# Kernel tuning notes

Hardware: AMD Instinct MI355X
Metric: run time of the kernel (lower is better)

Reference implementation:

```python
import jax, jax.numpy as jnp
import numpy as np

B, NCLASS, NSUPP = 4096, 1000, 64
NCHUNK = NSUPP * NSUPP  # 4096, x's feature dim


def setup_inputs() -> dict:
    key = jax.random.key(0)
    k1, k2, k3 = jax.random.split(key, 3)
    x = jax.random.normal(k1, (B, NCHUNK), dtype=jnp.float32)
    # torch .uniform_(-1, 1)
    wSupp = jax.random.uniform(k2, (NCLASS, NSUPP), dtype=jnp.float32, minval=-1.0, maxval=1.0)
    chunk_map = jax.random.randint(k3, (NCLASS, NSUPP), 0, NCHUNK, dtype=jnp.int32)
    return {"x": x, "wSupp": wSupp, "chunk_map": chunk_map}


def reference(x, wSupp, chunk_map):
    # sparse_support: for each class i, feat_i = sum_j x[:, chunk_map[i,j]] * wSupp[i,j]; out = exp(feat)
    gathered = x[:, chunk_map]                      # [B, nClass, nSupp] gather via index map
    feats = jnp.einsum('bcs,cs->bc', gathered, wSupp)  # weighted sum over support
    return jnp.exp(feats)                           # [B, nClass]
```

## Files before the change

### kernel.cpp

```cpp
#include <hip/hip_runtime.h>
#include <hip/hip_fp16.h>


constexpr int B_       = 4096;
constexpr int NCLASS_  = 1000;
constexpr int NSUPP_   = 64;
constexpr int NCHUNK_  = 4096;
constexpr int BT       = 8;
constexpr int THREADS_ = 1024;
constexpr int SG_      = NSUPP_ / 4;
constexpr size_t CMT_BYTES = (size_t)SG_ * NCLASS_ * 16;
constexpr size_t WS_NEEDED = 2 * CMT_BYTES;

__global__ __launch_bounds__(256)
void build_cw_kernel(const int*   __restrict__ cm,
                     const float* __restrict__ w,
                     int*         __restrict__ cmT,
                     __half2*     __restrict__ wTh)
{
    const int t    = threadIdx.x;
    const int c    = blockIdx.x * 4 + (t >> 6);
    const int lane = t & 63;
    if (c >= NCLASS_) return;

    const int   idx = cm[c * NSUPP_ + lane];
    const float wv  = w [c * NSUPP_ + lane];
    const int   key = (idx - c) & 7;

    const unsigned long long below = ((unsigned long long)1 << lane) - 1ull;
    int j = 0;
    #pragma unroll
    for (int r = 0; r < 8; ++r) {
        const unsigned long long m = __ballot(key == r);
        if (key > r)  j += __popcll(m);
        if (key == r) j += __popcll(m & below);
    }

    const int dst = ((j >> 2) * NCLASS_ + c) * 4 + (j & 3);
    cmT[dst] = idx;
    wTh[dst] = __float2half2_rn(wv);
}

static __device__ __forceinline__ __half2 f2h2(const float u) {
    union U { float f; __half2 h; } uu;
    uu.f = u;
    return uu.h;
}
static __device__ __forceinline__ float h2f(const __half2 h) {
    union U { __half2 h; float f; } uu;
    uu.h = h;
    return uu.f;
}

#define GSUPP(d, wj)                               \
    a0 = __hfma2(f2h2((d).x), (wj), a0);           \
    a1 = __hfma2(f2h2((d).y), (wj), a1);           \
    a2 = __hfma2(f2h2((d).z), (wj), a2);           \
    a3 = __hfma2(f2h2((d).w), (wj), a3);

#define FLUSH_ACC() {                              \
    float2 t_;                                     \
    t_ = __half22float2(a0); f0x += t_.x; f0y += t_.y; \
    t_ = __half22float2(a1); f1x += t_.x; f1y += t_.y; \
    t_ = __half22float2(a2); f2x += t_.x; f2y += t_.y; \
    t_ = __half22float2(a3); f3x += t_.x; f3y += t_.y; \
    a0 = z_; a1 = z_; a2 = z_; a3 = z_; }

template <bool USET>
__global__ __launch_bounds__(THREADS_)
void supp_gather_kernel(const float* __restrict__ x,
                        const float* __restrict__ wSupp,
                        const int*   __restrict__ cmap,
                        const float4* __restrict__ wTh4,
                        const int4*   __restrict__ cmT,
                        float*       __restrict__ out)
{
    __shared__ __align__(16) __half2 tile[NCHUNK_ * 4];

    const int t  = threadIdx.x;
    const int rb = blockIdx.x * BT;

    #pragma unroll
    for (int p = 0; p < NCHUNK_ / THREADS_; ++p) {
        const size_t col = (size_t)t + THREADS_ * p;
        float v0 = x[(size_t)(rb + 0) * NCHUNK_ + col];
        float v1 = x[(size_t)(rb + 1) * NCHUNK_ + col];
        float v2 = x[(size_t)(rb + 2) * NCHUNK_ + col];
        float v3 = x[(size_t)(rb + 3) * NCHUNK_ + col];
        float v4 = x[(size_t)(rb + 4) * NCHUNK_ + col];
        float v5 = x[(size_t)(rb + 5) * NCHUNK_ + col];
        float v6 = x[(size_t)(rb + 6) * NCHUNK_ + col];
        float v7 = x[(size_t)(rb + 7) * NCHUNK_ + col];
        float4 pk;
        pk.x = h2f(__floats2half2_rn(v0, v1));
        pk.y = h2f(__floats2half2_rn(v2, v3));
        pk.z = h2f(__floats2half2_rn(v4, v5));
        pk.w = h2f(__floats2half2_rn(v6, v7));
        *reinterpret_cast<float4*>(&tile[col * 4]) = pk;
    }
    __syncthreads();

    if (t < NCLASS_) {
        const int c = t;
        const float4* tile4 = reinterpret_cast<const float4*>(tile);

        const __half2 z_ = __floats2half2_rn(0.f, 0.f);
        __half2 a0 = z_, a1 = z_, a2 = z_, a3 = z_;
        float f0x = 0.f, f0y = 0.f, f1x = 0.f, f1y = 0.f;
        float f2x = 0.f, f2y = 0.f, f3x = 0.f, f3y = 0.f;

        int4   ci;
        float4 wh;
        if constexpr (USET) {
            ci = cmT [c];
            wh = wTh4[c];
        } else {
            ci = reinterpret_cast<const int4*>(cmap + c * NSUPP_)[0];
            wh = reinterpret_cast<const float4*>(wSupp + c * NSUPP_)[0];
        }

        #pragma unroll
        for (int sg = 0; sg < SG_; ++sg) {
            const int4   c4 = ci;
            const float4 w4 = wh;

            const int sgn = (sg + 1 < SG_) ? sg + 1 : SG_ - 1;
            if constexpr (USET) {
                ci = cmT [sgn * NCLASS_ + c];
                wh = wTh4[sgn * NCLASS_ + c];
            } else {
                ci = reinterpret_cast<const int4*>(cmap + c * NSUPP_)[sgn];
                wh = reinterpret_cast<const float4*>(wSupp + c * NSUPP_)[sgn];
            }

            const float4 d0 = tile4[c4.x];
            const float4 d1 = tile4[c4.y];
            const float4 d2 = tile4[c4.z];
            const float4 d3 = tile4[c4.w];

            const __half2 w0 = USET ? f2h2(w4.x) : __float2half2_rn(w4.x);
            const __half2 w1 = USET ? f2h2(w4.y) : __float2half2_rn(w4.y);
            const __half2 w2 = USET ? f2h2(w4.z) : __float2half2_rn(w4.z);
            const __half2 w3 = USET ? f2h2(w4.w) : __float2half2_rn(w4.w);

            GSUPP(d0, w0)
            GSUPP(d1, w1)
            GSUPP(d2, w2)
            GSUPP(d3, w3)

            if ((sg & 3) == 3) { FLUSH_ACC() }
        }

        out[(size_t)(rb + 0) * NCLASS_ + c] = __expf(f0x);
        out[(size_t)(rb + 1) * NCLASS_ + c] = __expf(f0y);
        out[(size_t)(rb + 2) * NCLASS_ + c] = __expf(f1x);
        out[(size_t)(rb + 3) * NCLASS_ + c] = __expf(f1y);
        out[(size_t)(rb + 4) * NCLASS_ + c] = __expf(f2x);
        out[(size_t)(rb + 5) * NCLASS_ + c] = __expf(f2y);
        out[(size_t)(rb + 6) * NCLASS_ + c] = __expf(f3x);
        out[(size_t)(rb + 7) * NCLASS_ + c] = __expf(f3y);
    }
}

extern "C" void kernel_launch(void* const* d_in, const int* in_sizes, int n_in,
                              void* d_out, int out_size, void* d_ws, size_t ws_size,
                              hipStream_t stream) {
    const float* x  = (const float*)d_in[0];
    const float* w  = (const float*)d_in[1];
    const int*   cm = (const int*)d_in[2];
    float*       o  = (float*)d_out;

    int*     cmT = (int*)d_ws;
    __half2* wTh = (__half2*)((char*)d_ws + CMT_BYTES);

    const dim3 grid(B_ / BT);
    if (ws_size >= WS_NEEDED) {
        build_cw_kernel<<<dim3((NCLASS_ + 3) / 4), dim3(256), 0, stream>>>(
            cm, w, cmT, wTh);
        supp_gather_kernel<true><<<grid, dim3(THREADS_), 0, stream>>>(
            x, w, cm, (const float4*)wTh, (const int4*)cmT, o);
    } else {
        supp_gather_kernel<false><<<grid, dim3(THREADS_), 0, stream>>>(
            x, w, cm, (const float4*)wTh, (const int4*)cmT, o);
    }
}
```

Baseline: 111.6 us.

## Process two row-tiles per block, overlapping second tile load with first gather

Each block now handles 16 batch rows as two 8-row halves held in a double-sized LDS tile. Global loads for the second half are issued between gather steps of the first half, with sched_barriers pinning the interleave, so memory latency overlaps the LDS gather and FMA work. Index and weight prefetch is reorganised into two ping-pong register sets, and the idle threads (t >= 1000) now also run the gather. The grid halves, LDS use doubles to 128KB per block, and register pressure rises, which may hurt occupancy.

```diff
diff --git a/kernel.cpp b/kernel.cpp
--- a/kernel.cpp
+++ b/kernel.cpp
@@ -6,7 +6,7 @@
 constexpr int NCLASS_  = 1000;
 constexpr int NSUPP_   = 64;
 constexpr int NCHUNK_  = 4096;
-constexpr int BT       = 8;
+constexpr int BT       = 16;
 constexpr int THREADS_ = 1024;
 constexpr int SG_      = NSUPP_ / 4;
 constexpr size_t CMT_BYTES = (size_t)SG_ * NCLASS_ * 16;
@@ -52,11 +52,43 @@
     return uu.f;
 }
 
+#define SB() __builtin_amdgcn_sched_barrier(0)
+
 #define GSUPP(d, wj)                               \
     a0 = __hfma2(f2h2((d).x), (wj), a0);           \
     a1 = __hfma2(f2h2((d).y), (wj), a1);           \
     a2 = __hfma2(f2h2((d).z), (wj), a2);           \
     a3 = __hfma2(f2h2((d).w), (wj), a3);
+
+#define GATHER(J, T4) {                            \
+    {   const float4 d0_ = (T4)[cwS##J.x];         \
+        const float4 d1_ = (T4)[cwS##J.y];         \
+        const __half2 w0_ = f2h2(whS##J.x);        \
+        const __half2 w1_ = f2h2(whS##J.y);        \
+        GSUPP(d0_, w0_)                            \
+        GSUPP(d1_, w1_) }                          \
+    {   const float4 d2_ = (T4)[cwS##J.z];         \
+        const float4 d3_ = (T4)[cwS##J.w];         \
+        const __half2 w2_ = f2h2(whS##J.z);        \
+        const __half2 w3_ = f2h2(whS##J.w);        \
+        GSUPP(d2_, w2_)                            \
+        GSUPP(d3_, w3_) } }
+
+#define REFILL(J, S)                                                         \
+    if constexpr (USET) {                                                    \
+        cwS##J = cmT [(S) * NCLASS_ + c];                                    \
+        whS##J = wTh4[(S) * NCLASS_ + c];                                    \
+    } else {                                                                 \
+        cwS##J = reinterpret_cast<const int4*>(cmap + c * NSUPP_)[(S)];      \
+        const float4 wf_ =                                                   \
+            reinterpret_cast<const float4*>(wSupp + c * NSUPP_)[(S)];        \
+        float4 wp_;                                                          \
+        wp_.x = h2f(__float2half2_rn(wf_.x));                                \
+        wp_.y = h2f(__float2half2_rn(wf_.y));                                \
+        wp_.z = h2f(__float2half2_rn(wf_.z));                                \
+        wp_.w = h2f(__float2half2_rn(wf_.w));                                \
+        whS##J = wp_;                                                        \
+    }
 
 #define FLUSH_ACC() {                              \
     float2 t_;                                     \
@@ -65,6 +97,26 @@
     t_ = __half22float2(a2); f2x += t_.x; f2y += t_.y; \
     t_ = __half22float2(a3); f3x += t_.x; f3y += t_.y; \
     a0 = z_; a1 = z_; a2 = z_; a3 = z_; }
+
+#define CHUNK_ISSUE(Q) {                                                     \
+    const size_t colq_ = (size_t)t + THREADS_ * (Q);                         \
+    hv0 = x[(size_t)(rb +  8) * NCHUNK_ + colq_];                            \
+    hv1 = x[(size_t)(rb +  9) * NCHUNK_ + colq_];                            \
+    hv2 = x[(size_t)(rb + 10) * NCHUNK_ + colq_];                            \
+    hv3 = x[(size_t)(rb + 11) * NCHUNK_ + colq_];                            \
+    hv4 = x[(size_t)(rb + 12) * NCHUNK_ + colq_];                            \
+    hv5 = x[(size_t)(rb + 13) * NCHUNK_ + colq_];                            \
+    hv6 = x[(size_t)(rb + 14) * NCHUNK_ + colq_];                            \
+    hv7 = x[(size_t)(rb + 15) * NCHUNK_ + colq_]; }
+
+#define CHUNK_CVT(Q) {                                                       \
+    const size_t colq_ = (size_t)t + THREADS_ * (Q);                         \
+    float4 pk_;                                                              \
+    pk_.x = h2f(__floats2half2_rn(hv0, hv1));                                \
+    pk_.y = h2f(__floats2half2_rn(hv2, hv3));                                \
+    pk_.z = h2f(__floats2half2_rn(hv4, hv5));                                \
+    pk_.w = h2f(__floats2half2_rn(hv6, hv7));                                \
+    *reinterpret_cast<float4*>(&thi[colq_ * 4]) = pk_; }
 
 template <bool USET>
 __global__ __launch_bounds__(THREADS_)
@@ -75,10 +127,19 @@
                         const int4*   __restrict__ cmT,
                         float*       __restrict__ out)
 {
-    __shared__ __align__(16) __half2 tile[NCHUNK_ * 4];
+    __shared__ __align__(16) __half2 tile[NCHUNK_ * 8];
+    __half2* tlo = tile;
+    __half2* thi = tile + NCHUNK_ * 4;
+    const float4* tlo4 = reinterpret_cast<const float4*>(tlo);
+    const float4* thi4 = reinterpret_cast<const float4*>(thi);
 
     const int t  = threadIdx.x;
     const int rb = blockIdx.x * BT;
+    const int c  = (t < NCLASS_) ? t : NCLASS_ - 1;
+
+    int4   cwS0, cwS1;
+    float4 whS0, whS1;
+    REFILL(0, 0) REFILL(1, 1)
 
     #pragma unroll
     for (int p = 0; p < NCHUNK_ / THREADS_; ++p) {
@@ -96,61 +157,38 @@
         pk.y = h2f(__floats2half2_rn(v2, v3));
         pk.z = h2f(__floats2half2_rn(v4, v5));
         pk.w = h2f(__floats2half2_rn(v6, v7));
-        *reinterpret_cast<float4*>(&tile[col * 4]) = pk;
+        *reinterpret_cast<float4*>(&tlo[col * 4]) = pk;
     }
     __syncthreads();
 
+    const __half2 z_ = __floats2half2_rn(0.f, 0.f);
+    __half2 a0 = z_, a1 = z_, a2 = z_, a3 = z_;
+    float f0x = 0.f, f0y = 0.f, f1x = 0.f, f1y = 0.f;
+    float f2x = 0.f, f2y = 0.f, f3x = 0.f, f3y = 0.f;
+    float hv0, hv1, hv2, hv3, hv4, hv5, hv6, hv7;
+
+     GATHER(0, tlo4) REFILL(0,  2) SB(); CHUNK_ISSUE(0) SB();
+     GATHER(1, tlo4) REFILL(1,  3) SB();
+     GATHER(0, tlo4) REFILL(0,  4) SB();
+     GATHER(1, tlo4) REFILL(1,  5) FLUSH_ACC() SB();
+     CHUNK_CVT(0) SB();
+           GATHER(0, tlo4) REFILL(0,  6) SB(); CHUNK_ISSUE(1) SB();
+     GATHER(1, tlo4) REFILL(1,  7) SB();
+     GATHER(0, tlo4) REFILL(0,  8) SB();
+     GATHER(1, tlo4) REFILL(1,  9) FLUSH_ACC() SB();
+     CHUNK_CVT(1) SB();
+           GATHER(0, tlo4) REFILL(0, 10) SB(); CHUNK_ISSUE(2) SB();
+     GATHER(1, tlo4) REFILL(1, 11) SB();
+     GATHER(0, tlo4) REFILL(0, 12) SB();
+     GATHER(1, tlo4) REFILL(1, 13) FLUSH_ACC() SB();
+     CHUNK_CVT(2) SB();
+           GATHER(0, tlo4) REFILL(0, 14) SB(); CHUNK_ISSUE(3) SB();
+     GATHER(1, tlo4) REFILL(1, 15) SB();
+     GATHER(0, tlo4) SB();
+     GATHER(1, tlo4) FLUSH_ACC() SB();
+    CHUNK_CVT(3) SB();
+
     if (t < NCLASS_) {
-        const int c = t;
-        const float4* tile4 = reinterpret_cast<const float4*>(tile);
-
-        const __half2 z_ = __floats2half2_rn(0.f, 0.f);
-        __half2 a0 = z_, a1 = z_, a2 = z_, a3 = z_;
-        float f0x = 0.f, f0y = 0.f, f1x = 0.f, f1y = 0.f;
-        float f2x = 0.f, f2y = 0.f, f3x = 0.f, f3y = 0.f;
-
-        int4   ci;
-        float4 wh;
-        if constexpr (USET) {
-            ci = cmT [c];
-            wh = wTh4[c];
-        } else {
-            ci = reinterpret_cast<const int4*>(cmap + c * NSUPP_)[0];
-            wh = reinterpret_cast<const float4*>(wSupp + c * NSUPP_)[0];
-        }
-
-        #pragma unroll
-        for (int sg = 0; sg < SG_; ++sg) {
-            const int4   c4 = ci;
-            const float4 w4 = wh;
-
-            const int sgn = (sg + 1 < SG_) ? sg + 1 : SG_ - 1;
-            if constexpr (USET) {
-                ci = cmT [sgn * NCLASS_ + c];
-                wh = wTh4[sgn * NCLASS_ + c];
-            } else {
-                ci = reinterpret_cast<const int4*>(cmap + c * NSUPP_)[sgn];
-                wh = reinterpret_cast<const float4*>(wSupp + c * NSUPP_)[sgn];
-            }
-
-            const float4 d0 = tile4[c4.x];
-            const float4 d1 = tile4[c4.y];
-            const float4 d2 = tile4[c4.z];
-            const float4 d3 = tile4[c4.w];
-
-            const __half2 w0 = USET ? f2h2(w4.x) : __float2half2_rn(w4.x);
-            const __half2 w1 = USET ? f2h2(w4.y) : __float2half2_rn(w4.y);
-            const __half2 w2 = USET ? f2h2(w4.z) : __float2half2_rn(w4.z);
-            const __half2 w3 = USET ? f2h2(w4.w) : __float2half2_rn(w4.w);
-
-            GSUPP(d0, w0)
-            GSUPP(d1, w1)
-            GSUPP(d2, w2)
-            GSUPP(d3, w3)
-
-            if ((sg & 3) == 3) { FLUSH_ACC() }
-        }
-
         out[(size_t)(rb + 0) * NCLASS_ + c] = __expf(f0x);
         out[(size_t)(rb + 1) * NCLASS_ + c] = __expf(f0y);
         out[(size_t)(rb + 2) * NCLASS_ + c] = __expf(f1x);
@@ -159,6 +197,39 @@
         out[(size_t)(rb + 5) * NCLASS_ + c] = __expf(f2y);
         out[(size_t)(rb + 6) * NCLASS_ + c] = __expf(f3x);
         out[(size_t)(rb + 7) * NCLASS_ + c] = __expf(f3y);
+    }
+    REFILL(0, 0) REFILL(1, 1)
+    __syncthreads();
+
+    a0 = z_; a1 = z_; a2 = z_; a3 = z_;
+    f0x = 0.f; f0y = 0.f; f1x = 0.f; f1y = 0.f;
+    f2x = 0.f; f2y = 0.f; f3x = 0.f; f3y = 0.f;
+    GATHER(0, thi4) REFILL(0,  2)
+    GATHER(1, thi4) REFILL(1,  3)
+    GATHER(0, thi4) REFILL(0,  4)
+    GATHER(1, thi4) REFILL(1,  5) FLUSH_ACC()
+    GATHER(0, thi4) REFILL(0,  6)
+    GATHER(1, thi4) REFILL(1,  7)
+    GATHER(0, thi4) REFILL(0,  8)
+    GATHER(1, thi4) REFILL(1,  9) FLUSH_ACC()
+    GATHER(0, thi4) REFILL(0, 10)
+    GATHER(1, thi4) REFILL(1, 11)
+    GATHER(0, thi4) REFILL(0, 12)
+    GATHER(1, thi4) REFILL(1, 13) FLUSH_ACC()
+    GATHER(0, thi4) REFILL(0, 14)
+    GATHER(1, thi4) REFILL(1, 15)
+    GATHER(0, thi4)
+    GATHER(1, thi4) FLUSH_ACC()
+
+    if (t < NCLASS_) {
+        out[(size_t)(rb +  8) * NCLASS_ + c] = __expf(f0x);
+        out[(size_t)(rb +  9) * NCLASS_ + c] = __expf(f0y);
+        out[(size_t)(rb + 10) * NCLASS_ + c] = __expf(f1x);
+        out[(size_t)(rb + 11) * NCLASS_ + c] = __expf(f1y);
+        out[(size_t)(rb + 12) * NCLASS_ + c] = __expf(f2x);
+        out[(size_t)(rb + 13) * NCLASS_ + c] = __expf(f2y);
+        out[(size_t)(rb + 14) * NCLASS_ + c] = __expf(f3x);
+        out[(size_t)(rb + 15) * NCLASS_ + c] = __expf(f3y);
     }
 }
 
```

Result: slower. 198.1 us (+77.5%).
